# Kernel tuning notes

Measured on AMD Instinct MI355X. Metric: run time of the kernel, lower is better.

## Reference

```python
import jax, jax.numpy as jnp
import numpy as np

HIDDEN = 2304
N_HEADS = 8
N_KV_HEADS = 4
HEAD_DIM = 256
SLIDING_WINDOW = 4096
QUERY_PRE_ATTN_SCALAR = 256.0
SOFTCAP = 50.0
ROPE_BASE = 10000.0


def setup_inputs() -> dict:
    key = jax.random.key(0)
    ks = jax.random.split(key, 6)
    B, S = 1, 4096
    scale = 0.02
    return {
        "hidden_states": jax.random.normal(ks[0], (B, S, HIDDEN), dtype=jnp.float32),
        "Wq": jax.random.normal(ks[1], (HIDDEN, N_HEADS * HEAD_DIM), dtype=jnp.float32) * scale,
        "Wk": jax.random.normal(ks[2], (HIDDEN, N_KV_HEADS * HEAD_DIM), dtype=jnp.float32) * scale,
        "Wv": jax.random.normal(ks[3], (HIDDEN, N_KV_HEADS * HEAD_DIM), dtype=jnp.float32) * scale,
        "Wo": jax.random.normal(ks[4], (N_HEADS * HEAD_DIM, HIDDEN), dtype=jnp.float32) * scale,
        "position_ids": jnp.arange(S, dtype=jnp.int64 if jax.config.jax_enable_x64 else jnp.int32)[None, :],
    }


def _rope_cos_sin(position_ids):
    # inv_freq: (head_dim//2,)
    inv_freq = 1.0 / (ROPE_BASE ** (jnp.arange(0, HEAD_DIM, 2, dtype=jnp.float32) / HEAD_DIM))
    freqs = position_ids.astype(jnp.float32)[..., None] * inv_freq[None, None, :]  # (B,S,hd/2)
    emb = jnp.concatenate([freqs, freqs], axis=-1)  # (B,S,hd)
    return jnp.cos(emb), jnp.sin(emb)


def _rotate_half(x):
    x1, x2 = jnp.split(x, 2, axis=-1)
    return jnp.concatenate([-x2, x1], axis=-1)


def reference(hidden_states, Wq, Wk, Wv, Wo, position_ids):
    B, S, _ = hidden_states.shape
    cos, sin = _rope_cos_sin(position_ids)  # (B,S,hd)
    cos = cos[:, None]  # (B,1,S,hd) broadcast over heads
    sin = sin[:, None]

    q = (hidden_states @ Wq).reshape(B, S, N_HEADS, HEAD_DIM).transpose(0, 2, 1, 3)
    k = (hidden_states @ Wk).reshape(B, S, N_KV_HEADS, HEAD_DIM).transpose(0, 2, 1, 3)
    v = (hidden_states @ Wv).reshape(B, S, N_KV_HEADS, HEAD_DIM).transpose(0, 2, 1, 3)

    q = q * cos + _rotate_half(q) * sin
    k = k * cos + _rotate_half(k) * sin

    # GQA: repeat kv heads to match query heads
    n_rep = N_HEADS // N_KV_HEADS
    k = jnp.repeat(k, n_rep, axis=1)  # (B,H,S,hd)
    v = jnp.repeat(v, n_rep, axis=1)

    scaling = QUERY_PRE_ATTN_SCALAR ** -0.5
    scores = jnp.einsum("bhqd,bhkd->bhqk", q, k) * scaling

    # attention logit softcapping
    scores = SOFTCAP * jnp.tanh(scores / SOFTCAP)

    # causal + sliding window mask
    qi = jnp.arange(S)[:, None]
    kj = jnp.arange(S)[None, :]
    mask = (kj <= qi) & (qi - kj < SLIDING_WINDOW)  # (S,S)
    scores = jnp.where(mask[None, None], scores, jnp.asarray(-1e30, scores.dtype))

    attn = jax.nn.softmax(scores, axis=-1)
    ctx = jnp.einsum("bhqk,bhkd->bhqd", attn, v)  # (B,H,S,hd)
    ctx = ctx.transpose(0, 2, 1, 3).reshape(B, S, N_HEADS * HEAD_DIM)
    return ctx @ Wo
```

## Files before the change

### kernel.cpp

```cpp
#include <hip/hip_runtime.h>
#include <cstdint>
#include <cstddef>

typedef unsigned short u16;
typedef short bf16x8 __attribute__((ext_vector_type(8)));
typedef float f32x4 __attribute__((ext_vector_type(4)));

#define S_LEN 4096
#define HID   2304
#define NH    8
#define NKV   4
#define HD    256
#define QD    2048
#define KD    1024
#define QKVW  4096
#define CHT   16
#define SLOTS_PER_HEAD 288

__device__ __forceinline__ u16 f2b(float f) {
    union { float f; uint32_t u; } v; v.f = f;
    uint32_t r = (v.u + 0x7FFFu + ((v.u >> 16) & 1u)) >> 16;
    return (u16)r;
}
__device__ __forceinline__ float b2f(u16 u) {
    union { uint32_t u; float f; } v; v.u = ((uint32_t)u) << 16;
    return v.f;
}

__device__ __forceinline__ void glds16(const void* g, void* l) {
    __builtin_amdgcn_global_load_lds(
        (__attribute__((address_space(1))) void*)(const_cast<void*>(g)),
        (__attribute__((address_space(3))) void*)l, 16, 0, 0);
}

__device__ __forceinline__ int slot_base(int qt) {
    int a = qt >> 3, b = qt & 7;
    return (a + 1) * (4 * a + b);
}

__device__ __forceinline__ float softcap_p(float s) {
    float u = s * 0.00125f;
    u = fminf(fmaxf(u, -0.53f), 0.53f);
    float u2 = u * u;
    float t50 = u * (50.0f + u2 * (-16.6666667f + 6.66666667f * u2));
    return __expf(t50);
}

__global__ __launch_bounds__(256) void cvt_h(const float* __restrict__ in, u16* __restrict__ out, int n4) {
    int id = blockIdx.x * 256 + threadIdx.x;
    if (id >= n4) return;
    float4 v = ((const float4*)in)[id];
    uint2 o;
    o.x = (uint32_t)f2b(v.x) | ((uint32_t)f2b(v.y) << 16);
    o.y = (uint32_t)f2b(v.z) | ((uint32_t)f2b(v.w) << 16);
    ((uint2*)out)[id] = o;
}

__device__ __forceinline__ void twcvt_body(const float* __restrict__ W, u16* __restrict__ out,
                                           int K, int N, int ldo, int n0, int k0) {
    __shared__ float T[64][68];
    const int t = threadIdx.x;
    for (int i = 0; i < 4; i++) {
        int id = i * 256 + t;
        int r = id >> 4, c4 = id & 15;
        float4 v = *(const float4*)(W + (size_t)(k0 + r) * N + n0 + c4 * 4);
        *(float4*)(&T[r][c4 * 4]) = v;
    }
    __syncthreads();
    for (int i = 0; i < 4; i++) {
        int id = i * 256 + t;
        int rn = id >> 4, c4 = id & 15;
        u16 a = f2b(T[c4 * 4 + 0][rn]);
        u16 b = f2b(T[c4 * 4 + 1][rn]);
        u16 c = f2b(T[c4 * 4 + 2][rn]);
        u16 d = f2b(T[c4 * 4 + 3][rn]);
        uint2 o;
        o.x = (uint32_t)a | ((uint32_t)b << 16);
        o.y = (uint32_t)c | ((uint32_t)d << 16);
        *(uint2*)(out + (size_t)(n0 + rn) * ldo + k0 + c4 * 4) = o;
    }
}

__global__ __launch_bounds__(256) void twcvt(const float* __restrict__ W, u16* __restrict__ out,
                                             int K, int N, int ldo) {
    twcvt_body(W, out, K, N, ldo, blockIdx.x * 64, blockIdx.y * 64);
}

__global__ __launch_bounds__(256) void twcvt_qkv(const float* __restrict__ Wq,
                                                 const float* __restrict__ Wk,
                                                 const float* __restrict__ Wv,
                                                 u16* __restrict__ out) {
    const int z = blockIdx.z;
    const float* W = (z == 0) ? Wq : (z == 1) ? Wk : Wv;
    const int N = (z == 0) ? QD : KD;
    const int n0 = blockIdx.x * 64;
    if (n0 >= N) return;
    u16* ob = out + ((z == 0) ? 0 : (z == 1) ? (size_t)QD * HID : (size_t)(QD + KD) * HID);
    twcvt_body(W, ob, HID, N, HID, n0, blockIdx.y * 64);
}

template<int BF16_OUT>
__global__ __launch_bounds__(256, 2) void gemm_bt(const u16* __restrict__ A, const u16* __restrict__ B,
                                                  void* __restrict__ Cp, int M, int N, int K) {
    const int tid  = threadIdx.x;
    const int wv = tid >> 6, lane = tid & 63;
    const int quad = lane >> 4, m16 = lane & 15;
    const int m0 = blockIdx.y * 128, n0 = blockIdx.x * 128;
    const int wm = (wv & 1) * 64, wn = (wv >> 1) * 64;
    __shared__ __align__(16) u16 As[128 * 32];
    __shared__ __align__(16) u16 Bs[128 * 32];
    int s0i = (wv * 2) * 64 + lane, s1i = s0i + 64;
    int row0 = s0i >> 2, c0 = (s0i & 3) ^ (row0 & 3);
    int row1 = s1i >> 2, c1 = (s1i & 3) ^ (row1 & 3);
    const u16* pA0 = A + (size_t)(m0 + row0) * K + c0 * 8;
    const u16* pA1 = A + (size_t)(m0 + row1) * K + c1 * 8;
    const u16* pB0 = B + (size_t)(n0 + row0) * K + c0 * 8;
    const u16* pB1 = B + (size_t)(n0 + row1) * K + c1 * 8;
    u16* lA0 = &As[(wv * 2 + 0) * 512]; u16* lA1 = &As[(wv * 2 + 1) * 512];
    u16* lB0 = &Bs[(wv * 2 + 0) * 512]; u16* lB1 = &Bs[(wv * 2 + 1) * 512];

    const f32x4 z4 = {0.f, 0.f, 0.f, 0.f};
    f32x4 acc00 = z4, acc01 = z4, acc02 = z4, acc03 = z4;
    f32x4 acc10 = z4, acc11 = z4, acc12 = z4, acc13 = z4;
    f32x4 acc20 = z4, acc21 = z4, acc22 = z4, acc23 = z4;
    f32x4 acc30 = z4, acc31 = z4, acc32 = z4, acc33 = z4;

    const int sw = quad ^ (m16 & 3);
    const u16* ra0 = &As[(wm + 0 * 16 + m16) * 32 + (sw << 3)];
    const u16* ra1 = &As[(wm + 1 * 16 + m16) * 32 + (sw << 3)];
    const u16* ra2 = &As[(wm + 2 * 16 + m16) * 32 + (sw << 3)];
    const u16* ra3 = &As[(wm + 3 * 16 + m16) * 32 + (sw << 3)];
    const u16* rb0 = &Bs[(wn + 0 * 16 + m16) * 32 + (sw << 3)];
    const u16* rb1 = &Bs[(wn + 1 * 16 + m16) * 32 + (sw << 3)];
    const u16* rb2 = &Bs[(wn + 2 * 16 + m16) * 32 + (sw << 3)];
    const u16* rb3 = &Bs[(wn + 3 * 16 + m16) * 32 + (sw << 3)];

    for (int k0 = 0; k0 < K; k0 += 32) {
        __syncthreads();
        glds16(pA0 + k0, lA0);
        glds16(pA1 + k0, lA1);
        glds16(pB0 + k0, lB0);
        glds16(pB1 + k0, lB1);
        __syncthreads();
        bf16x8 af0 = *(const bf16x8*)ra0, af1 = *(const bf16x8*)ra1;
        bf16x8 af2 = *(const bf16x8*)ra2, af3 = *(const bf16x8*)ra3;
        bf16x8 bf0 = *(const bf16x8*)rb0, bf1 = *(const bf16x8*)rb1;
        bf16x8 bf2 = *(const bf16x8*)rb2, bf3 = *(const bf16x8*)rb3;
        acc00 = __builtin_amdgcn_mfma_f32_16x16x32_bf16(af0, bf0, acc00, 0, 0, 0);
        acc01 = __builtin_amdgcn_mfma_f32_16x16x32_bf16(af0, bf1, acc01, 0, 0, 0);
        acc02 = __builtin_amdgcn_mfma_f32_16x16x32_bf16(af0, bf2, acc02, 0, 0, 0);
        acc03 = __builtin_amdgcn_mfma_f32_16x16x32_bf16(af0, bf3, acc03, 0, 0, 0);
        acc10 = __builtin_amdgcn_mfma_f32_16x16x32_bf16(af1, bf0, acc10, 0, 0, 0);
        acc11 = __builtin_amdgcn_mfma_f32_16x16x32_bf16(af1, bf1, acc11, 0, 0, 0);
        acc12 = __builtin_amdgcn_mfma_f32_16x16x32_bf16(af1, bf2, acc12, 0, 0, 0);
        acc13 = __builtin_amdgcn_mfma_f32_16x16x32_bf16(af1, bf3, acc13, 0, 0, 0);
        acc20 = __builtin_amdgcn_mfma_f32_16x16x32_bf16(af2, bf0, acc20, 0, 0, 0);
        acc21 = __builtin_amdgcn_mfma_f32_16x16x32_bf16(af2, bf1, acc21, 0, 0, 0);
        acc22 = __builtin_amdgcn_mfma_f32_16x16x32_bf16(af2, bf2, acc22, 0, 0, 0);
        acc23 = __builtin_amdgcn_mfma_f32_16x16x32_bf16(af2, bf3, acc23, 0, 0, 0);
        acc30 = __builtin_amdgcn_mfma_f32_16x16x32_bf16(af3, bf0, acc30, 0, 0, 0);
        acc31 = __builtin_amdgcn_mfma_f32_16x16x32_bf16(af3, bf1, acc31, 0, 0, 0);
        acc32 = __builtin_amdgcn_mfma_f32_16x16x32_bf16(af3, bf2, acc32, 0, 0, 0);
        acc33 = __builtin_amdgcn_mfma_f32_16x16x32_bf16(af3, bf3, acc33, 0, 0, 0);
    }

#define STORE_TILE(I, J, ACC)                                              \
    {                                                                      \
        _Pragma("unroll")                                                  \
        for (int r = 0; r < 4; r++) {                                      \
            int row = m0 + wm + (I) * 16 + quad * 4 + r;                   \
            int col = n0 + wn + (J) * 16 + m16;                            \
            float v = (ACC)[r];                                            \
            if (BF16_OUT) ((u16*)Cp)[(size_t)row * N + col] = f2b(v);      \
            else          ((float*)Cp)[(size_t)row * N + col] = v;         \
        }                                                                  \
    }
    STORE_TILE(0, 0, acc00) STORE_TILE(0, 1, acc01) STORE_TILE(0, 2, acc02) STORE_TILE(0, 3, acc03)
    STORE_TILE(1, 0, acc10) STORE_TILE(1, 1, acc11) STORE_TILE(1, 2, acc12) STORE_TILE(1, 3, acc13)
    STORE_TILE(2, 0, acc20) STORE_TILE(2, 1, acc21) STORE_TILE(2, 2, acc22) STORE_TILE(2, 3, acc23)
    STORE_TILE(3, 0, acc30) STORE_TILE(3, 1, acc31) STORE_TILE(3, 2, acc32) STORE_TILE(3, 3, acc33)
#undef STORE_TILE
}

__global__ __launch_bounds__(256) void rope_k(const u16* __restrict__ QKV, const int* __restrict__ pos,
                                              u16* __restrict__ Qb, u16* __restrict__ Kb) {
    int id = blockIdx.x * 256 + threadIdx.x;
    const int NQ = S_LEN * NH * 128;
    const u16* src; u16* dst;
    int s, j;
    if (id < NQ) {
        s = id >> 10; int rem = id & 1023; int h = rem >> 7; j = rem & 127;
        src = QKV + (size_t)s * QKVW + h * 256;
        dst = Qb + (size_t)s * QD + h * 256;
    } else {
        int id2 = id - NQ;
        s = id2 >> 9; int rem = id2 & 511; int kvh = rem >> 7; j = rem & 127;
        src = QKV + (size_t)s * QKVW + QD + kvh * 256;
        dst = Kb + (size_t)s * KD + kvh * 256;
    }
    float p = (float)pos[s];
    float invf = expf(-0.07195578429985445f * (float)j);
    float ang = p * invf;
    float sn, cs;
    sincosf(ang, &sn, &cs);
    float x1 = b2f(src[j]), x2 = b2f(src[j + 128]);
    dst[j]       = f2b(x1 * cs - x2 * sn);
    dst[j + 128] = f2b(x2 * cs + x1 * sn);
}

__global__ __launch_bounds__(256) void vtrans(const u16* __restrict__ QKV, u16* __restrict__ Vt) {
    const int s0 = blockIdx.x * 64, d0 = blockIdx.y * 64;
    __shared__ u16 T[64][72];
    const int t = threadIdx.x;
    for (int i = 0; i < 2; i++) {
        int id = i * 256 + t;
        int r = id >> 3, c = id & 7;
        uint4 v = *(const uint4*)(QKV + (size_t)(s0 + r) * QKVW + (QD + KD) + d0 + c * 8);
        *(uint4*)(&T[r][c * 8]) = v;
    }
    __syncthreads();
    for (int i = 0; i < 2; i++) {
        int id = i * 256 + t;
        int r = id >> 3, c = id & 7;
        union { u16 u[8]; uint4 v; } o;
        for (int jj = 0; jj < 8; jj++) o.u[jj] = T[c * 8 + jj][r];
        *(uint4*)(Vt + (size_t)(d0 + r) * S_LEN + s0 + c * 8) = o.v;
    }
}

__global__ __launch_bounds__(256, 3) void attn_part(const u16* __restrict__ Qb, const u16* __restrict__ Kb,
                                                    const u16* __restrict__ Vt,
                                                    u16* __restrict__ Part, float* __restrict__ Lpart) {
    const int tid  = threadIdx.x;
    const int wv = tid >> 6, lane = tid & 63;
    const int quad = lane >> 4, m16 = lane & 15;
    const int qt = blockIdx.x, h = blockIdx.y, ch = blockIdx.z;
    const int n_kvt = 2 * qt + 2;
    const int t0 = ch * CHT;
    if (t0 >= n_kvt) return;
    const int t1 = min(t0 + CHT, n_kvt);
    const int kvh = h >> 1;
    const int q0 = qt * 64;
    const int slot = h * SLOTS_PER_HEAD + slot_base(qt) + ch;

    __shared__ __align__(16) u16 Kl[2][32 * 256];
    __shared__ __align__(16) u16 Vl[256 * 32];
    __shared__ __align__(16) u16 Pl[4][16 * 32];

    int kOff[4], vOff[4];
#pragma unroll
    for (int i = 0; i < 4; i++) {
        int s = (wv * 4 + i) * 64 + lane;
        int kv = s >> 5, c = (s & 31) ^ (kv & 7);
        kOff[i] = kv * KD + c * 8;
        int d = s >> 2, cc = (s & 3) ^ ((d >> 1) & 3);
        vOff[i] = d * S_LEN + cc * 8;
    }
    const u16* Kbase = Kb + kvh * 256;
    const u16* Vbase = Vt + (size_t)(kvh * 256) * S_LEN;

    bf16x8 qf[8];
    {
        const u16* qp = Qb + (size_t)(q0 + wv * 16 + m16) * QD + h * 256 + quad * 8;
#pragma unroll
        for (int ks = 0; ks < 8; ks++) qf[ks] = *(const bf16x8*)(qp + ks * 32);
    }
    float li[4] = {0.f, 0.f, 0.f, 0.f};
    f32x4 o[16];
#pragma unroll
    for (int i = 0; i < 16; i++) o[i] = (f32x4){0.f, 0.f, 0.f, 0.f};

#pragma unroll
    for (int i = 0; i < 4; i++)
        glds16(Kbase + kOff[i] + t0 * (32 * KD), &Kl[0][(wv * 4 + i) * 512]);

    for (int kt = t0; kt < t1; kt++) {
        const int cur = (kt - t0) & 1, nxt = cur ^ 1;
        __syncthreads();
#pragma unroll
        for (int i = 0; i < 4; i++)
            glds16(Vbase + vOff[i] + kt * 32, &Vl[(wv * 4 + i) * 512]);
        if (kt + 1 < t1) {
#pragma unroll
            for (int i = 0; i < 4; i++)
                glds16(Kbase + kOff[i] + (kt + 1) * (32 * KD), &Kl[nxt][(wv * 4 + i) * 512]);
        }
        f32x4 s[2];
#pragma unroll
        for (int nt = 0; nt < 2; nt++) {
            f32x4 a = (f32x4){0.f, 0.f, 0.f, 0.f};
            int kr = nt * 16 + m16;
            int sw = kr & 7;
#pragma unroll
            for (int ks = 0; ks < 8; ks++) {
                int c = ks * 4 + quad;
                bf16x8 kf = *(const bf16x8*)(&Kl[cur][kr * 256 + ((c ^ sw) << 3)]);
                a = __builtin_amdgcn_mfma_f32_16x16x32_bf16(qf[ks], kf, a, 0, 0, 0);
            }
            s[nt] = a;
        }
        const int kvb = kt * 32;
        u16* Pw = &Pl[wv][0];
#pragma unroll
        for (int nt = 0; nt < 2; nt++)
#pragma unroll
            for (int r = 0; r < 4; r++) {
                float p = softcap_p(s[nt][r]);
                int kvg = kvb + nt * 16 + m16;
                int qg  = q0 + wv * 16 + quad * 4 + r;
                p = (kvg > qg) ? 0.f : p;
                li[r] += p;
                int m = quad * 4 + r;
                int c = 2 * nt + (m16 >> 3);
                int off = m16 & 7;
                Pw[m * 32 + ((c ^ ((m >> 1) & 3)) << 3) + off] = f2b(p);
            }
        bf16x8 pf = *(const bf16x8*)(&Pw[m16 * 32 + ((quad ^ ((m16 >> 1) & 3)) << 3)]);
        __syncthreads();
#pragma unroll
        for (int dt = 0; dt < 16; dt++) {
            int d = dt * 16 + m16;
            bf16x8 vf = *(const bf16x8*)(&Vl[d * 32 + ((quad ^ ((d >> 1) & 3)) << 3)]);
            o[dt] = __builtin_amdgcn_mfma_f32_16x16x32_bf16(pf, vf, o[dt], 0, 0, 0);
        }
    }
    u16* Pp = Part + (size_t)slot * (64 * 256);
#pragma unroll
    for (int dt = 0; dt < 16; dt++)
#pragma unroll
        for (int r = 0; r < 4; r++)
            Pp[(wv * 16 + quad * 4 + r) * 256 + dt * 16 + m16] = f2b(o[dt][r]);
#pragma unroll
    for (int r = 0; r < 4; r++) {
        float l = li[r];
        l += __shfl_xor(l, 1); l += __shfl_xor(l, 2);
        l += __shfl_xor(l, 4); l += __shfl_xor(l, 8);
        if (m16 == 0) Lpart[slot * 64 + wv * 16 + quad * 4 + r] = l;
    }
}

__global__ __launch_bounds__(256) void attn_combine(const u16* __restrict__ Part,
                                                    const float* __restrict__ Lpart,
                                                    u16* __restrict__ Ctx) {
    const int qt = blockIdx.x, h = blockIdx.y;
    const int nch = (qt >> 3) + 1;
    const int slot0 = h * SLOTS_PER_HEAD + slot_base(qt);
    const int t = threadIdx.x;
    const int q0 = qt * 64;
    __shared__ float linv[64];
    if (t < 64) {
        float l = 0.f;
        for (int c = 0; c < nch; c++) l += Lpart[(slot0 + c) * 64 + t];
        linv[t] = 1.f / l;
    }
    __syncthreads();
    const u16* P0 = Part + (size_t)slot0 * (64 * 256);
    for (int i = 0; i < 8; i++) {
        int idx = i * 256 + t;
        int row = idx >> 5, c8 = idx & 31;
        float acc[8] = {0.f,0.f,0.f,0.f,0.f,0.f,0.f,0.f};
        for (int c = 0; c < nch; c++) {
            uint4 v = *(const uint4*)(P0 + (size_t)c * (64 * 256) + row * 256 + c8 * 8);
            uint32_t w[4] = {v.x, v.y, v.z, v.w};
            for (int k = 0; k < 4; k++) {
                acc[k * 2]     += b2f((u16)(w[k] & 0xFFFF));
                acc[k * 2 + 1] += b2f((u16)(w[k] >> 16));
            }
        }
        float iv = linv[row];
        uint4 ov;
        uint32_t* op = (uint32_t*)&ov;
        for (int k = 0; k < 4; k++)
            op[k] = (uint32_t)f2b(acc[k * 2] * iv) | ((uint32_t)f2b(acc[k * 2 + 1] * iv) << 16);
        *(uint4*)(Ctx + (size_t)(q0 + row) * QD + h * 256 + c8 * 8) = ov;
    }
}

extern "C" void kernel_launch(void* const* d_in, const int* in_sizes, int n_in,
                              void* d_out, int out_size, void* d_ws, size_t ws_size,
                              hipStream_t stream) {
    const float* H  = (const float*)d_in[0];
    const float* Wq = (const float*)d_in[1];
    const float* Wk = (const float*)d_in[2];
    const float* Wv = (const float*)d_in[3];
    const float* Wo = (const float*)d_in[4];
    const int* pos  = (const int*)d_in[5];
    float* out = (float*)d_out;

    char* ws = (char*)d_ws;
    size_t off = 0;
    u16* Hb     = (u16*)(ws + off); off += (size_t)S_LEN * HID * 2;
    u16* Wqkvt  = (u16*)(ws + off); off += (size_t)QKVW * HID * 2;
    u16* Wot    = (u16*)(ws + off); off += (size_t)HID * QD * 2;
    u16* QKVraw = (u16*)(ws + off); off += (size_t)S_LEN * QKVW * 2;
    u16* Qb     = (u16*)(ws + off); off += (size_t)S_LEN * QD * 2;
    u16* Kb     = (u16*)(ws + off); off += (size_t)S_LEN * KD * 2;
    u16* Vt     = (u16*)(ws + off); off += (size_t)KD * S_LEN * 2;
    u16* Ctx    = (u16*)(ws + off); off += (size_t)S_LEN * QD * 2;
    u16* Part   = (u16*)(ws + off);  off += (size_t)NH * SLOTS_PER_HEAD * 64 * 256 * 2;
    float* Lprt = (float*)(ws + off); off += (size_t)NH * SLOTS_PER_HEAD * 64 * 4;

    cvt_h<<<dim3((S_LEN * HID / 4 + 255) / 256), dim3(256), 0, stream>>>(H, Hb, S_LEN * HID / 4);
    twcvt_qkv<<<dim3(32, HID / 64, 3), dim3(256), 0, stream>>>(Wq, Wk, Wv, Wqkvt);
    twcvt<<<dim3(HID / 64, QD / 64), dim3(256), 0, stream>>>(Wo, Wot, QD, HID, QD);
    gemm_bt<1><<<dim3(QKVW / 128, S_LEN / 128), dim3(256), 0, stream>>>(Hb, Wqkvt, QKVraw, S_LEN, QKVW, HID);
    rope_k<<<dim3((S_LEN * NH * 128 + S_LEN * NKV * 128) / 256), dim3(256), 0, stream>>>(QKVraw, pos, Qb, Kb);
    vtrans<<<dim3(S_LEN / 64, KD / 64), dim3(256), 0, stream>>>(QKVraw, Vt);
    attn_part<<<dim3(64, NH, 8), dim3(256), 0, stream>>>(Qb, Kb, Vt, Part, Lprt);
    attn_combine<<<dim3(64, NH), dim3(256), 0, stream>>>(Part, Lprt, Ctx);
    gemm_bt<0><<<dim3(HID / 128, S_LEN / 128), dim3(256), 0, stream>>>(Ctx, Wot, out, S_LEN, HID, QD);
}
```

Measured before the change: 488.5 us.

## Repartition attention waves into 2x2 query/key-dim tiles with shared P buffer

Each wave in the attention partial kernel now handles 32 query rows against 16 keys for QK^T and 32 query rows against 128 head-dim columns for PV, instead of 16 rows against the full tile. This lets each K and V fragment loaded from LDS feed two MFMAs, halving the LDS fragment reads per MFMA. The P tile is shared across waves through one buffer, and row sums are reduced with shuffles plus a small LDS step. It also adds s_setprio around MFMA bursts and lowers the occupancy hint from 3 to 2, trading occupancy for more registers.

```diff
diff --git a/kernel.cpp b/kernel.cpp
--- a/kernel.cpp
+++ b/kernel.cpp
@@ -228,12 +228,13 @@
     }
 }
 
-__global__ __launch_bounds__(256, 3) void attn_part(const u16* __restrict__ Qb, const u16* __restrict__ Kb,
+__global__ __launch_bounds__(256, 2) void attn_part(const u16* __restrict__ Qb, const u16* __restrict__ Kb,
                                                     const u16* __restrict__ Vt,
                                                     u16* __restrict__ Part, float* __restrict__ Lpart) {
     const int tid  = threadIdx.x;
     const int wv = tid >> 6, lane = tid & 63;
     const int quad = lane >> 4, m16 = lane & 15;
+    const int qh = wv & 1, dh = wv >> 1;
     const int qt = blockIdx.x, h = blockIdx.y, ch = blockIdx.z;
     const int n_kvt = 2 * qt + 2;
     const int t0 = ch * CHT;
@@ -245,7 +246,8 @@
 
     __shared__ __align__(16) u16 Kl[2][32 * 256];
     __shared__ __align__(16) u16 Vl[256 * 32];
-    __shared__ __align__(16) u16 Pl[4][16 * 32];
+    __shared__ __align__(16) u16 Pl[64 * 32];
+    __shared__ float Lred[64];
 
     int kOff[4], vOff[4];
 #pragma unroll
@@ -259,20 +261,26 @@
     const u16* Kbase = Kb + kvh * 256;
     const u16* Vbase = Vt + (size_t)(kvh * 256) * S_LEN;
 
-    bf16x8 qf[8];
-    {
-        const u16* qp = Qb + (size_t)(q0 + wv * 16 + m16) * QD + h * 256 + quad * 8;
-#pragma unroll
-        for (int ks = 0; ks < 8; ks++) qf[ks] = *(const bf16x8*)(qp + ks * 32);
-    }
-    float li[4] = {0.f, 0.f, 0.f, 0.f};
-    f32x4 o[16];
-#pragma unroll
-    for (int i = 0; i < 16; i++) o[i] = (f32x4){0.f, 0.f, 0.f, 0.f};
+    bf16x8 qf[2][8];
+#pragma unroll
+    for (int qs = 0; qs < 2; qs++) {
+        const u16* qp = Qb + (size_t)(q0 + qh * 32 + qs * 16 + m16) * QD + h * 256 + quad * 8;
+#pragma unroll
+        for (int ks = 0; ks < 8; ks++) qf[qs][ks] = *(const bf16x8*)(qp + ks * 32);
+    }
+    float li[2] = {0.f, 0.f};
+    f32x4 o[2][8];
+#pragma unroll
+    for (int qs = 0; qs < 2; qs++)
+#pragma unroll
+        for (int j = 0; j < 8; j++) o[qs][j] = (f32x4){0.f, 0.f, 0.f, 0.f};
 
 #pragma unroll
     for (int i = 0; i < 4; i++)
         glds16(Kbase + kOff[i] + t0 * (32 * KD), &Kl[0][(wv * 4 + i) * 512]);
+
+    const int pkey = m16 & 6;
+    const int ksw  = m16 & 7;
 
     for (int kt = t0; kt < t1; kt++) {
         const int cur = (kt - t0) & 1, nxt = cur ^ 1;
@@ -285,57 +293,71 @@
             for (int i = 0; i < 4; i++)
                 glds16(Kbase + kOff[i] + (kt + 1) * (32 * KD), &Kl[nxt][(wv * 4 + i) * 512]);
         }
-        f32x4 s[2];
-#pragma unroll
-        for (int nt = 0; nt < 2; nt++) {
-            f32x4 a = (f32x4){0.f, 0.f, 0.f, 0.f};
-            int kr = nt * 16 + m16;
-            int sw = kr & 7;
+        f32x4 st[2] = {(f32x4){0.f,0.f,0.f,0.f}, (f32x4){0.f,0.f,0.f,0.f}};
+        {
+            const u16* krow = &Kl[cur][(dh * 16 + m16) * 256];
+            __builtin_amdgcn_s_setprio(1);
 #pragma unroll
             for (int ks = 0; ks < 8; ks++) {
-                int c = ks * 4 + quad;
-                bf16x8 kf = *(const bf16x8*)(&Kl[cur][kr * 256 + ((c ^ sw) << 3)]);
-                a = __builtin_amdgcn_mfma_f32_16x16x32_bf16(qf[ks], kf, a, 0, 0, 0);
+                bf16x8 kf = *(const bf16x8*)(krow + (((ks * 4 + quad) ^ ksw) << 3));
+                st[0] = __builtin_amdgcn_mfma_f32_16x16x32_bf16(kf, qf[0][ks], st[0], 0, 0, 0);
+                st[1] = __builtin_amdgcn_mfma_f32_16x16x32_bf16(kf, qf[1][ks], st[1], 0, 0, 0);
             }
-            s[nt] = a;
-        }
-        const int kvb = kt * 32;
-        u16* Pw = &Pl[wv][0];
-#pragma unroll
-        for (int nt = 0; nt < 2; nt++)
-#pragma unroll
-            for (int r = 0; r < 4; r++) {
-                float p = softcap_p(s[nt][r]);
-                int kvg = kvb + nt * 16 + m16;
-                int qg  = q0 + wv * 16 + quad * 4 + r;
-                p = (kvg > qg) ? 0.f : p;
-                li[r] += p;
-                int m = quad * 4 + r;
-                int c = 2 * nt + (m16 >> 3);
-                int off = m16 & 7;
-                Pw[m * 32 + ((c ^ ((m >> 1) & 3)) << 3) + off] = f2b(p);
-            }
-        bf16x8 pf = *(const bf16x8*)(&Pw[m16 * 32 + ((quad ^ ((m16 >> 1) & 3)) << 3)]);
+            __builtin_amdgcn_s_setprio(0);
+        }
+        const int kvr0 = kt * 32 + dh * 16 + quad * 4;
+#pragma unroll
+        for (int qs = 0; qs < 2; qs++) {
+            const int qg = q0 + qh * 32 + qs * 16 + m16;
+            float p0 = (kvr0 + 0 > qg) ? 0.f : softcap_p(st[qs][0]);
+            float p1 = (kvr0 + 1 > qg) ? 0.f : softcap_p(st[qs][1]);
+            float p2 = (kvr0 + 2 > qg) ? 0.f : softcap_p(st[qs][2]);
+            float p3 = (kvr0 + 3 > qg) ? 0.f : softcap_p(st[qs][3]);
+            li[qs] += (p0 + p1) + (p2 + p3);
+            uint2 w;
+            w.x = (uint32_t)f2b(p0) | ((uint32_t)f2b(p1) << 16);
+            w.y = (uint32_t)f2b(p2) | ((uint32_t)f2b(p3) << 16);
+            const int qrow = qh * 32 + qs * 16 + m16;
+            *(uint2*)(&Pl[qrow * 32 + (((dh * 4 + quad) ^ pkey) << 2)]) = w;
+        }
         __syncthreads();
-#pragma unroll
-        for (int dt = 0; dt < 16; dt++) {
-            int d = dt * 16 + m16;
+        bf16x8 pf[2];
+#pragma unroll
+        for (int qs = 0; qs < 2; qs++) {
+            const int qrow = qh * 32 + qs * 16 + m16;
+            pf[qs] = *(const bf16x8*)(&Pl[qrow * 32 + (((2 * quad) ^ pkey) << 2)]);
+        }
+        __builtin_amdgcn_s_setprio(1);
+#pragma unroll
+        for (int j = 0; j < 8; j++) {
+            const int d = dh * 128 + j * 16 + m16;
             bf16x8 vf = *(const bf16x8*)(&Vl[d * 32 + ((quad ^ ((d >> 1) & 3)) << 3)]);
-            o[dt] = __builtin_amdgcn_mfma_f32_16x16x32_bf16(pf, vf, o[dt], 0, 0, 0);
-        }
+            o[0][j] = __builtin_amdgcn_mfma_f32_16x16x32_bf16(pf[0], vf, o[0][j], 0, 0, 0);
+            o[1][j] = __builtin_amdgcn_mfma_f32_16x16x32_bf16(pf[1], vf, o[1][j], 0, 0, 0);
+        }
+        __builtin_amdgcn_s_setprio(0);
     }
     u16* Pp = Part + (size_t)slot * (64 * 256);
 #pragma unroll
-    for (int dt = 0; dt < 16; dt++)
-#pragma unroll
-        for (int r = 0; r < 4; r++)
-            Pp[(wv * 16 + quad * 4 + r) * 256 + dt * 16 + m16] = f2b(o[dt][r]);
-#pragma unroll
-    for (int r = 0; r < 4; r++) {
-        float l = li[r];
-        l += __shfl_xor(l, 1); l += __shfl_xor(l, 2);
-        l += __shfl_xor(l, 4); l += __shfl_xor(l, 8);
-        if (m16 == 0) Lpart[slot * 64 + wv * 16 + quad * 4 + r] = l;
+    for (int qs = 0; qs < 2; qs++)
+#pragma unroll
+        for (int j = 0; j < 8; j++)
+#pragma unroll
+            for (int r = 0; r < 4; r++)
+                Pp[(qh * 32 + qs * 16 + quad * 4 + r) * 256 + dh * 128 + j * 16 + m16] = f2b(o[qs][j][r]);
+#pragma unroll
+    for (int qs = 0; qs < 2; qs++) {
+        li[qs] += __shfl_xor(li[qs], 16);
+        li[qs] += __shfl_xor(li[qs], 32);
+    }
+    if (dh == 0 && quad == 0) {
+        Lred[qh * 32 + m16]      = li[0];
+        Lred[qh * 32 + 16 + m16] = li[1];
+    }
+    __syncthreads();
+    if (dh == 1 && quad == 0) {
+        Lpart[slot * 64 + qh * 32 + m16]      = li[0] + Lred[qh * 32 + m16];
+        Lpart[slot * 64 + qh * 32 + 16 + m16] = li[1] + Lred[qh * 32 + 16 + m16];
     }
 }
 
```

After: 510.0 us. 1.04x slower.
